# Performance work log

Hardware: AMD Instinct MI355X
Metric: run time of the kernel (lower is better)

## Reference

```python
import jax, jax.numpy as jnp
import numpy as np


def setup_inputs() -> dict:
    key = jax.random.key(0)
    k1, k2, k3, k4 = jax.random.split(key, 4)
    B, T, C, H = 8, 2048, 1024, 64
    x = jax.random.normal(k1, (B, T, C), dtype=jnp.float32)
    # nn.Linear weights, stored as (in, out) for x @ W
    Wk = jax.random.normal(k2, (C, H), dtype=jnp.float32) * (C ** -0.5)
    Wq = jax.random.normal(k3, (C, H), dtype=jnp.float32) * (C ** -0.5)
    Wv = jax.random.normal(k4, (C, H), dtype=jnp.float32) * (C ** -0.5)
    return {"x": x, "Wk": Wk, "Wq": Wq, "Wv": Wv}


def reference(x, Wk, Wq, Wv):
    B, T, C = x.shape
    k = x @ Wk  # [B,T,H]
    q = x @ Wq  # [B,T,H]
    v = x @ Wv  # [B,T,H]
    # NOTE: original scales by C**-0.5 (full embed dim), not head_size**-0.5
    wei = jnp.einsum("bth,bsh->bts", q, k) * (C ** -0.5)  # [B,T,T]
    causal = jnp.tril(jnp.ones((T, T), dtype=bool))
    wei = jnp.where(causal, wei, -jnp.inf)
    wei = jax.nn.softmax(wei, axis=-1)
    # dropout is identity in eval/reference mode
    out = jnp.einsum("bts,bsh->bth", wei, v)  # [B,T,H]
    return out
```

## Files before the change

kernel.cpp:

```cpp
#include <hip/hip_runtime.h>
#include <hip/hip_bf16.h>
#include <math.h>

#define B_ 8
#define T_ 2048
#define C_ 1024
#define H_ 64
#define M_ (B_*T_)

typedef __attribute__((ext_vector_type(8))) short short8;
typedef __attribute__((ext_vector_type(4))) float f32x4;
typedef unsigned int u32;

__device__ __forceinline__ unsigned short f2bf(float f) {
    u32 u = __builtin_bit_cast(u32, f);
    u += 0x7FFFu + ((u >> 16) & 1u);
    return (unsigned short)(u >> 16);
}

__device__ __forceinline__ void gl2lds16(const void* g, void* l) {
    __builtin_amdgcn_global_load_lds(
        (const __attribute__((address_space(1))) u32*)g,
        (__attribute__((address_space(3))) u32*)l, 16, 0, 0);
}

__global__ __launch_bounds__(256) void wconv(
    const float* __restrict__ Wk, const float* __restrict__ Wq,
    const float* __restrict__ Wv, unsigned short* __restrict__ wb)
{
    __shared__ unsigned short lt[64][64];
    const int mat = blockIdx.x >> 4;
    const int k0  = (blockIdx.x & 15) * 64;
    const float* src = (mat == 0) ? Wk : (mat == 1 ? Wq : Wv);
    const float sc = (mat == 1) ? 0.03125f : 1.0f;
    const int tid = threadIdx.x;

    for (int it = 0; it < 16; ++it) {
        int idx = it * 256 + tid;
        int r = idx >> 6, cn = idx & 63;
        lt[cn][r] = f2bf(src[(size_t)(k0 + r) * H_ + cn] * sc);
    }
    __syncthreads();
    for (int g = 0; g < 2; ++g) {
        int n  = g * 32 + (tid >> 3);
        int kp = tid & 7;
        int ng = mat * 64 + n;
        short8 v = *reinterpret_cast<const short8*>(&lt[n][kp * 8]);
        char* dst = (char*)wb + (size_t)ng * 2048 + (k0 >> 6) * 128
                  + ((kp * 16) ^ ((ng & 7) << 4));
        *reinterpret_cast<short8*>(dst) = v;
    }
}

__global__ __launch_bounds__(256, 2) void qkv_mm(
    const float* __restrict__ x, const unsigned short* __restrict__ wb,
    unsigned short* __restrict__ kb, unsigned short* __restrict__ qb,
    unsigned short* __restrict__ vT)
{
    __shared__ __align__(16) unsigned short Ws[2][96 * 64];

    const int tid  = threadIdx.x;
    const int wid  = tid >> 6;
    const int lane = tid & 63;
    const int lr   = lane & 15;
    const int lg   = lane >> 4;
    const int mt   = blockIdx.x >> 1;
    const int bn   = blockIdx.x & 1;
    const int m0   = mt * 64;
    const int n0   = bn * 96;

    const float* xrow = x + (size_t)(m0 + wid * 16 + lr) * C_ + lg * 8;

    f32x4 acc[6];
    for (int c = 0; c < 6; ++c) acc[c] = (f32x4){0.f, 0.f, 0.f, 0.f};

    float4 xa = *reinterpret_cast<const float4*>(xrow);
    float4 xb2 = *reinterpret_cast<const float4*>(xrow + 4);
    float4 xc = *reinterpret_cast<const float4*>(xrow + 32);
    float4 xd = *reinterpret_cast<const float4*>(xrow + 36);
    for (int p = 0; p < 3; ++p) {
        int c = p * 256 + tid;
        gl2lds16((const char*)wb + (size_t)(n0 + (c >> 3)) * 2048 + (c & 7) * 16,
                 (char*)&Ws[0][0] + c * 16);
    }

    for (int t = 0; t < 16; ++t) {
        __syncthreads();
        float4 na, nb, nc, nd;
        if (t < 15) {
            const float* xn = xrow + (t + 1) * 64;
            na = *reinterpret_cast<const float4*>(xn);
            nb = *reinterpret_cast<const float4*>(xn + 4);
            nc = *reinterpret_cast<const float4*>(xn + 32);
            nd = *reinterpret_cast<const float4*>(xn + 36);
            int buf = (t + 1) & 1;
            for (int p = 0; p < 3; ++p) {
                int c = p * 256 + tid;
                gl2lds16((const char*)wb + (size_t)(n0 + (c >> 3)) * 2048
                             + (size_t)(t + 1) * 128 + (c & 7) * 16,
                         (char*)&Ws[buf][0] + c * 16);
            }
        }

        short8 af0, af1;
        af0[0] = (short)f2bf(xa.x); af0[1] = (short)f2bf(xa.y);
        af0[2] = (short)f2bf(xa.z); af0[3] = (short)f2bf(xa.w);
        af0[4] = (short)f2bf(xb2.x); af0[5] = (short)f2bf(xb2.y);
        af0[6] = (short)f2bf(xb2.z); af0[7] = (short)f2bf(xb2.w);
        af1[0] = (short)f2bf(xc.x); af1[1] = (short)f2bf(xc.y);
        af1[2] = (short)f2bf(xc.z); af1[3] = (short)f2bf(xc.w);
        af1[4] = (short)f2bf(xd.x); af1[5] = (short)f2bf(xd.y);
        af1[6] = (short)f2bf(xd.z); af1[7] = (short)f2bf(xd.w);

        const char* wbuf = (const char*)&Ws[t & 1][0];
        #pragma unroll
        for (int kc = 0; kc < 2; ++kc) {
            short8 afc = kc ? af1 : af0;
            #pragma unroll
            for (int ct = 0; ct < 6; ++ct) {
                int n = ct * 16 + lr;
                short8 bf = *reinterpret_cast<const short8*>(
                    wbuf + n * 128 + ((kc * 64 + lg * 16) ^ ((n & 7) << 4)));
                acc[ct] = __builtin_amdgcn_mfma_f32_16x16x32_bf16(afc, bf, acc[ct], 0, 0, 0);
            }
        }
        xa = na; xb2 = nb; xc = nc; xd = nd;
    }

    for (int ct = 0; ct < 6; ++ct) {
        int ng = n0 + ct * 16 + lr;
        int col = ng & 63;
        for (int i = 0; i < 4; ++i) {
            int m = m0 + wid * 16 + lg * 4 + i;
            unsigned short val = f2bf(acc[ct][i]);
            if (ng < 64)       kb[(size_t)m * H_ + col] = val;
            else if (ng < 128) qb[(size_t)m * H_ + col] = val;
            else               vT[((size_t)(m >> 11) * H_ + col) * T_ + (m & (T_ - 1))] = val;
        }
    }
}

__global__ __launch_bounds__(256, 2) void attn4(
    const unsigned short* __restrict__ kb,
    const unsigned short* __restrict__ qb,
    const unsigned short* __restrict__ vT,
    float* __restrict__ out)
{
    __shared__ __align__(16) unsigned short Ps[4][16][72];
    __shared__ float Om[4][16][64];
    __shared__ float Mv[4][16], Lv[4][16], Fac[4][16], InvL[16];

    const int tid  = threadIdx.x;
    const int wid  = tid >> 6;
    const int lane = tid & 63;
    const int lr   = lane & 15;
    const int lg   = lane >> 4;
    const int b    = blockIdx.y;
    const int bx   = blockIdx.x;
    const int tile = (bx & 1) ? (127 - (bx >> 1)) : (bx >> 1);
    const int q0   = tile * 16;
    const int nsteps = (tile >> 2) + 1;
    const size_t base = (size_t)b * T_ * H_;
    const unsigned short* vTb = vT + (size_t)b * H_ * T_;

    short8 qf[2];
    #pragma unroll
    for (int kc = 0; kc < 2; ++kc)
        qf[kc] = *reinterpret_cast<const short8*>(
            qb + base + (size_t)(q0 + lr) * H_ + kc * 32 + lg * 8);

    f32x4 o[4];
    float mrun[4], lrun[4];
    for (int dt = 0; dt < 4; ++dt) o[dt] = (f32x4){0.f, 0.f, 0.f, 0.f};
    for (int i = 0; i < 4; ++i) { mrun[i] = -INFINITY; lrun[i] = 0.f; }

    for (int s = wid; s < nsteps; s += 4) {
        const int kv0 = s * 64;

        short8 kf[2][4];
        #pragma unroll
        for (int kc = 0; kc < 2; ++kc)
            #pragma unroll
            for (int kt = 0; kt < 4; ++kt)
                kf[kc][kt] = *reinterpret_cast<const short8*>(
                    kb + base + (size_t)(kv0 + kt * 16 + lr) * H_ + kc * 32 + lg * 8);

        f32x4 sv4[4];
        for (int kt = 0; kt < 4; ++kt) sv4[kt] = (f32x4){0.f, 0.f, 0.f, 0.f};
        #pragma unroll
        for (int kc = 0; kc < 2; ++kc)
            #pragma unroll
            for (int kt = 0; kt < 4; ++kt)
                sv4[kt] = __builtin_amdgcn_mfma_f32_16x16x32_bf16(qf[kc], kf[kc][kt], sv4[kt], 0, 0, 0);

        short8 vf[2][4];
        #pragma unroll
        for (int kc = 0; kc < 2; ++kc)
            #pragma unroll
            for (int dt = 0; dt < 4; ++dt)
                vf[kc][dt] = *reinterpret_cast<const short8*>(
                    vTb + (size_t)(dt * 16 + lr) * T_ + kv0 + kc * 32 + lg * 8);

        const bool need_mask = (s == nsteps - 1);

        for (int i = 0; i < 4; ++i) {
            int row = q0 + lg * 4 + i;
            float sv[4];
            float mx = -INFINITY;
            if (need_mask) {
                for (int kt = 0; kt < 4; ++kt) {
                    int key = kv0 + kt * 16 + lr;
                    float v = (key <= row) ? sv4[kt][i] : -INFINITY;
                    sv[kt] = v;
                    mx = fmaxf(mx, v);
                }
            } else {
                for (int kt = 0; kt < 4; ++kt) {
                    sv[kt] = sv4[kt][i];
                    mx = fmaxf(mx, sv[kt]);
                }
            }
            for (int d = 8; d; d >>= 1) mx = fmaxf(mx, __shfl_xor(mx, d));
            float mn  = fmaxf(mrun[i], mx);
            float fac = __expf(mrun[i] - mn);
            float rs  = 0.f;
            for (int kt = 0; kt < 4; ++kt) {
                float p = __expf(sv[kt] - mn);
                rs += p;
                Ps[wid][lg * 4 + i][kt * 16 + lr] = f2bf(p);
            }
            for (int d = 8; d; d >>= 1) rs += __shfl_xor(rs, d);
            lrun[i] = lrun[i] * fac + rs;
            mrun[i] = mn;
            for (int dt = 0; dt < 4; ++dt)
                o[dt][i] *= fac;
        }

        #pragma unroll
        for (int kc = 0; kc < 2; ++kc) {
            short8 pf = *reinterpret_cast<const short8*>(&Ps[wid][lr][kc * 32 + lg * 8]);
            #pragma unroll
            for (int dt = 0; dt < 4; ++dt)
                o[dt] = __builtin_amdgcn_mfma_f32_16x16x32_bf16(pf, vf[kc][dt], o[dt], 0, 0, 0);
        }
    }

    for (int dt = 0; dt < 4; ++dt)
        for (int i = 0; i < 4; ++i)
            Om[wid][lg * 4 + i][dt * 16 + lr] = o[dt][i];
    if (lr == 0)
        for (int i = 0; i < 4; ++i) {
            Mv[wid][lg * 4 + i] = mrun[i];
            Lv[wid][lg * 4 + i] = lrun[i];
        }
    __syncthreads();
    if (tid < 16) {
        float M = Mv[0][tid];
        for (int w = 1; w < 4; ++w) M = fmaxf(M, Mv[w][tid]);
        float L = 0.f;
        for (int w = 0; w < 4; ++w) {
            float f = __expf(Mv[w][tid] - M);
            Fac[w][tid] = f;
            L += Lv[w][tid] * f;
        }
        InvL[tid] = 1.0f / L;
    }
    __syncthreads();
    for (int e = 0; e < 4; ++e) {
        int idx = e * 256 + tid;
        int row = idx >> 6, d = idx & 63;
        float v = 0.f;
        for (int w = 0; w < 4; ++w) v += Om[w][row][d] * Fac[w][row];
        out[base + (size_t)(q0 + row) * H_ + d] = v * InvL[row];
    }
}

extern "C" void kernel_launch(void* const* d_in, const int* in_sizes, int n_in,
                              void* d_out, int out_size, void* d_ws, size_t ws_size,
                              hipStream_t stream) {
    const float* x  = (const float*)d_in[0];
    const float* Wk = (const float*)d_in[1];
    const float* Wq = (const float*)d_in[2];
    const float* Wv = (const float*)d_in[3];
    float* out = (float*)d_out;

    unsigned short* kb = (unsigned short*)d_ws;
    unsigned short* qb = kb + (size_t)M_ * H_;
    unsigned short* vT = qb + (size_t)M_ * H_;
    unsigned short* wb = vT + (size_t)M_ * H_;

    wconv<<<48, 256, 0, stream>>>(Wk, Wq, Wv, wb);
    qkv_mm<<<512, 256, 0, stream>>>(x, wb, kb, qb, vT);
    attn4<<<dim3(128, B_), 256, 0, stream>>>(kb, qb, vT, out);
}
```

Before: 179.5 us.

## Stage K/V tiles into swizzled LDS via async loads with per-wave double buffering

Replaces direct global-to-register K and V fragment loads in the attention kernel with asynchronous global_load_lds copies into a per-wave LDS slice. K is double-buffered, V is single-buffered and restaged after the PV MFMAs. Manual vmcnt waits let the next tile's loads overlap with the current tile's compute. Rows use an XOR swizzle to avoid LDS bank conflicts, and the Om reduction buffer is aliased onto the staging buffer. The larger LDS footprint (about 96KB plus extras) and the dropped min-blocks launch bound may reduce occupancy, and the hand-tuned waitcnt counts are fragile.

Result: slower. 191.2 us (+6.5%).

```diff
diff --git a/kernel.cpp b/kernel.cpp
--- a/kernel.cpp
+++ b/kernel.cpp
@@ -140,14 +140,14 @@
     }
 }
 
-__global__ __launch_bounds__(256, 2) void attn4(
+__global__ __launch_bounds__(256) void attn6(
     const unsigned short* __restrict__ kb,
     const unsigned short* __restrict__ qb,
     const unsigned short* __restrict__ vT,
     float* __restrict__ out)
 {
+    __shared__ __align__(16) char kvbuf[4][24576];
     __shared__ __align__(16) unsigned short Ps[4][16][72];
-    __shared__ float Om[4][16][64];
     __shared__ float Mv[4][16], Lv[4][16], Fac[4][16], InvL[16];
 
     const int tid  = threadIdx.x;
@@ -159,9 +159,11 @@
     const int bx   = blockIdx.x;
     const int tile = (bx & 1) ? (127 - (bx >> 1)) : (bx >> 1);
     const int q0   = tile * 16;
-    const int nsteps = (tile >> 2) + 1;
+    const int nst  = (tile >> 2) + 1;
     const size_t base = (size_t)b * T_ * H_;
-    const unsigned short* vTb = vT + (size_t)b * H_ * T_;
+    const char* kbyte = (const char*)(kb + base);
+    const char* vbyte = (const char*)(vT + (size_t)b * H_ * T_);
+    char* slice = kvbuf[wid];
 
     short8 qf[2];
     #pragma unroll
@@ -174,40 +176,61 @@
     for (int dt = 0; dt < 4; ++dt) o[dt] = (f32x4){0.f, 0.f, 0.f, 0.f};
     for (int i = 0; i < 4; ++i) { mrun[i] = -INFINITY; lrun[i] = 0.f; }
 
-    for (int s = wid; s < nsteps; s += 4) {
+    auto stageK = [&](int buf, int kv0) {
+        const char* ks = kbyte + kv0 * 128;
+        char* dst = slice + buf * 8192;
+        #pragma unroll
+        for (int i = 0; i < 8; ++i) {
+            int c = i * 64 + lane;
+            int row = c >> 3, colB = (c & 7) * 16;
+            gl2lds16(ks + row * 128 + (colB ^ ((row & 7) << 4)), dst + c * 16);
+        }
+    };
+    auto stageV = [&](int kv0) {
+        const char* vs = vbyte + kv0 * 2;
+        char* dst = slice + 16384;
+        #pragma unroll
+        for (int i = 0; i < 8; ++i) {
+            int c = i * 64 + lane;
+            int row = c >> 3, colB = (c & 7) * 16;
+            gl2lds16(vs + (size_t)row * 4096 + (colB ^ ((row & 7) << 4)), dst + c * 16);
+        }
+    };
+
+    int s = wid, cur = 0;
+    if (s < nst) { stageK(0, s * 64); stageV(s * 64); }
+
+    for (; s < nst; s += 4) {
         const int kv0 = s * 64;
-
-        short8 kf[2][4];
-        #pragma unroll
-        for (int kc = 0; kc < 2; ++kc)
-            #pragma unroll
-            for (int kt = 0; kt < 4; ++kt)
-                kf[kc][kt] = *reinterpret_cast<const short8*>(
-                    kb + base + (size_t)(kv0 + kt * 16 + lr) * H_ + kc * 32 + lg * 8);
-
+        const bool more = (s + 4) < nst;
+
+        asm volatile("s_waitcnt vmcnt(8)" ::: "memory");
+        __builtin_amdgcn_sched_barrier(0);
+        if (more) stageK(cur ^ 1, kv0 + 256);
+
+        const char* kt_base = slice + cur * 8192;
         f32x4 sv4[4];
+        #pragma unroll
         for (int kt = 0; kt < 4; ++kt) sv4[kt] = (f32x4){0.f, 0.f, 0.f, 0.f};
         #pragma unroll
-        for (int kc = 0; kc < 2; ++kc)
-            #pragma unroll
-            for (int kt = 0; kt < 4; ++kt)
-                sv4[kt] = __builtin_amdgcn_mfma_f32_16x16x32_bf16(qf[kc], kf[kc][kt], sv4[kt], 0, 0, 0);
-
-        short8 vf[2][4];
-        #pragma unroll
-        for (int kc = 0; kc < 2; ++kc)
-            #pragma unroll
-            for (int dt = 0; dt < 4; ++dt)
-                vf[kc][dt] = *reinterpret_cast<const short8*>(
-                    vTb + (size_t)(dt * 16 + lr) * T_ + kv0 + kc * 32 + lg * 8);
-
-        const bool need_mask = (s == nsteps - 1);
-
+        for (int kc = 0; kc < 2; ++kc) {
+            #pragma unroll
+            for (int kt = 0; kt < 4; ++kt) {
+                int row = kt * 16 + lr;
+                short8 kf = *reinterpret_cast<const short8*>(
+                    kt_base + row * 128 + ((kc * 64 + lg * 16) ^ ((row & 7) << 4)));
+                sv4[kt] = __builtin_amdgcn_mfma_f32_16x16x32_bf16(qf[kc], kf, sv4[kt], 0, 0, 0);
+            }
+        }
+
+        const bool need_mask = (s == nst - 1);
+        #pragma unroll
         for (int i = 0; i < 4; ++i) {
             int row = q0 + lg * 4 + i;
             float sv[4];
             float mx = -INFINITY;
             if (need_mask) {
+                #pragma unroll
                 for (int kt = 0; kt < 4; ++kt) {
                     int key = kv0 + kt * 16 + lr;
                     float v = (key <= row) ? sv4[kt][i] : -INFINITY;
@@ -215,6 +238,7 @@
                     mx = fmaxf(mx, v);
                 }
             } else {
+                #pragma unroll
                 for (int kt = 0; kt < 4; ++kt) {
                     sv[kt] = sv4[kt][i];
                     mx = fmaxf(mx, sv[kt]);
@@ -224,6 +248,7 @@
             float mn  = fmaxf(mrun[i], mx);
             float fac = __expf(mrun[i] - mn);
             float rs  = 0.f;
+            #pragma unroll
             for (int kt = 0; kt < 4; ++kt) {
                 float p = __expf(sv[kt] - mn);
                 rs += p;
@@ -232,19 +257,34 @@
             for (int d = 8; d; d >>= 1) rs += __shfl_xor(rs, d);
             lrun[i] = lrun[i] * fac + rs;
             mrun[i] = mn;
+            #pragma unroll
             for (int dt = 0; dt < 4; ++dt)
                 o[dt][i] *= fac;
         }
 
+        asm volatile("s_waitcnt vmcnt(8)" ::: "memory");
+        __builtin_amdgcn_sched_barrier(0);
+
+        const char* vt_base = slice + 16384;
         #pragma unroll
         for (int kc = 0; kc < 2; ++kc) {
             short8 pf = *reinterpret_cast<const short8*>(&Ps[wid][lr][kc * 32 + lg * 8]);
             #pragma unroll
-            for (int dt = 0; dt < 4; ++dt)
-                o[dt] = __builtin_amdgcn_mfma_f32_16x16x32_bf16(pf, vf[kc][dt], o[dt], 0, 0, 0);
-        }
-    }
-
+            for (int dt = 0; dt < 4; ++dt) {
+                int row = dt * 16 + lr;
+                short8 vf = *reinterpret_cast<const short8*>(
+                    vt_base + row * 128 + ((kc * 64 + lg * 16) ^ ((row & 7) << 4)));
+                o[dt] = __builtin_amdgcn_mfma_f32_16x16x32_bf16(pf, vf, o[dt], 0, 0, 0);
+            }
+        }
+
+        __builtin_amdgcn_sched_barrier(0);
+        if (more) stageV(kv0 + 256);
+        cur ^= 1;
+    }
+
+    __syncthreads();
+    float (*Om)[16][64] = (float (*)[16][64])kvbuf;
     for (int dt = 0; dt < 4; ++dt)
         for (int i = 0; i < 4; ++i)
             Om[wid][lg * 4 + i][dt * 16 + lr] = o[dt][i];
@@ -291,5 +331,5 @@
 
     wconv<<<48, 256, 0, stream>>>(Wk, Wq, Wv, wb);
     qkv_mm<<<512, 256, 0, stream>>>(x, wb, kb, qb, vT);
-    attn4<<<dim3(128, B_), 256, 0, stream>>>(kb, qb, vT, out);
-}
+    attn6<<<dim3(128, B_), 256, 0, stream>>>(kb, qb, vT, out);
+}
```
